# Performance work log

Measured on AMD Instinct MI355X. Metric: run time of the kernel, lower is better.

Reference implementation:

```python
import jax, jax.numpy as jnp
import numpy as np

B, T, I, H, L = 32, 512, 1024, 1024, 2

def setup_inputs() -> dict:
    key = jax.random.key(0)
    ks = jax.random.split(key, 5)
    x = jax.random.normal(ks[0], (B, T, I), dtype=jnp.float32)
    # nn.Linear weight layout: [out_features, in_features] = [4H, in+H]
    scale0 = (6.0 / (4 * H + I + H)) ** 0.5  # xavier uniform bound
    scale1 = (6.0 / (4 * H + H + H)) ** 0.5
    W0 = jax.random.uniform(ks[1], (4 * H, I + H), minval=-scale0, maxval=scale0, dtype=jnp.float32)
    W1 = jax.random.uniform(ks[2], (4 * H, H + H), minval=-scale1, maxval=scale1, dtype=jnp.float32)
    # bias: zeros, with forget-gate slice (first H) set to 1, per reset_parameters
    b = jnp.zeros((4 * H,), dtype=jnp.float32).at[:H].set(1.0)
    return {"x": x, "W0": W0, "b0": b, "W1": W1, "b1": b}

def _cell(x_in, h_prev, c_prev, W, b):
    # combined:[B, in+H] @ W.T -> [B, 4H]
    gates = jnp.concatenate([x_in, h_prev], axis=1) @ W.T + b
    f, i, g, o = jnp.split(gates, 4, axis=1)
    f = jax.nn.sigmoid(f)
    i = jax.nn.sigmoid(i)
    g = jnp.tanh(g)
    o = jax.nn.sigmoid(o)
    c_next = f * c_prev + i * g
    h_next = o * jnp.tanh(c_next)
    return h_next, c_next

def reference(x, W0, b0, W1, b1):
    Ws = (W0, W1)
    bs = (b0, b1)
    x_t_major = jnp.transpose(x, (1, 0, 2))  # [T, B, I]
    h0 = jnp.zeros((L, B, H), dtype=x.dtype)
    c0 = jnp.zeros((L, B, H), dtype=x.dtype)

    def step(carry, x_t):
        h, c = carry
        inp = x_t
        hs, cs = [], []
        for l in range(L):
            h_new, c_new = _cell(inp, h[l], c[l], Ws[l], bs[l])
            hs.append(h_new)
            cs.append(c_new)
            inp = h_new  # dropout=0 -> identity between layers
        return (jnp.stack(hs), jnp.stack(cs)), inp

    (h_n, c_n), outs = jax.lax.scan(step, (h0, c0), x_t_major)
    outputs = jnp.transpose(outs, (1, 0, 2))  # batch_first
    return outputs, h_n, c_n
```

## Files before the change

### kernel.cpp

```cpp
#include <hip/hip_runtime.h>
#include <hip/hip_bf16.h>
#include <cstdint>
#include <cstddef>


typedef unsigned short ush;
typedef short bf16x8 __attribute__((ext_vector_type(8)));
typedef float f32x4 __attribute__((ext_vector_type(4)));
typedef int i32x4 __attribute__((ext_vector_type(4)));
typedef unsigned long long u64;

#define TT 512
#define NA 64
#define NB 128
#define RING 8

__device__ __forceinline__ ush f2bf(float f) {
  __hip_bfloat16 h = __float2bfloat16(f);
  return *reinterpret_cast<ush*>(&h);
}
__device__ __forceinline__ float sigm(float x) { return 1.f / (1.f + __expf(-x)); }

__device__ __forceinline__ unsigned int aload(const unsigned int* p) {
  return __hip_atomic_load(p, __ATOMIC_RELAXED, __HIP_MEMORY_SCOPE_AGENT);
}
__device__ __forceinline__ void astore(unsigned int* p, unsigned int v) {
  __hip_atomic_store(p, v, __ATOMIC_RELAXED, __HIP_MEMORY_SCOPE_AGENT);
}

__global__ __launch_bounds__(256) void cast_w1k(const float* __restrict__ W,
                                                ush* __restrict__ Wb, int off) {
  int j = blockIdx.x;
  int k = threadIdx.x * 4;
  float4 v = *(const float4*)(W + (size_t)j * 2048 + off + k);
  ushort4 o;
  o.x = f2bf(v.x); o.y = f2bf(v.y); o.z = f2bf(v.z); o.w = f2bf(v.w);
  *(ushort4*)(Wb + (size_t)j * 1024 + k) = o;
}

__global__ __launch_bounds__(256) void swz0(const float* __restrict__ W,
                                            ush* __restrict__ D) {
  int n = blockIdx.x * 256 + threadIdx.x;
  int lane = n & 63, ch = (n >> 6) & 15, w = (n >> 10) & 7, i = n >> 13;
  int l15 = lane & 15, quad = lane >> 4, g = w & 3, kh = w >> 2;
  int row = g * 1024 + i * 16 + l15;
  int col = 1024 + kh * 512 + ch * 32 + quad * 8;
  const float* src = W + (size_t)row * 2048 + col;
  float4 v0 = ((const float4*)src)[0];
  float4 v1 = ((const float4*)src)[1];
  ushort4 o0, o1;
  o0.x = f2bf(v0.x); o0.y = f2bf(v0.y); o0.z = f2bf(v0.z); o0.w = f2bf(v0.w);
  o1.x = f2bf(v1.x); o1.y = f2bf(v1.y); o1.z = f2bf(v1.z); o1.w = f2bf(v1.w);
  *(ushort4*)(D + (size_t)n * 8) = o0;
  *(ushort4*)(D + (size_t)n * 8 + 4) = o1;
}

__global__ __launch_bounds__(256) void swz1(const float* __restrict__ W,
                                            ush* __restrict__ D) {
  int n = blockIdx.x * 256 + threadIdx.x;
  int lane = n & 63, ch = (n >> 6) & 15, w = (n >> 10) & 7, j = n >> 13;
  int l15 = lane & 15, quad = lane >> 4, rh = w & 1, kq = w >> 1;
  int r32 = rh * 16 + l15;
  int row = (r32 >> 3) * 1024 + j * 8 + (r32 & 7);
  int col = kq * 512 + ch * 32 + quad * 8;
  const float* src = W + (size_t)row * 2048 + col;
  float4 v0 = ((const float4*)src)[0];
  float4 v1 = ((const float4*)src)[1];
  ushort4 o0, o1;
  o0.x = f2bf(v0.x); o0.y = f2bf(v0.y); o0.z = f2bf(v0.z); o0.w = f2bf(v0.w);
  o1.x = f2bf(v1.x); o1.y = f2bf(v1.y); o1.z = f2bf(v1.z); o1.w = f2bf(v1.w);
  *(ushort4*)(D + (size_t)n * 8) = o0;
  *(ushort4*)(D + (size_t)n * 8 + 4) = o1;
}

__global__ __launch_bounds__(256) void zeroreg(uint4* __restrict__ p) {
  p[blockIdx.x * 256 + threadIdx.x] = uint4{0, 0, 0, 0};
}

__global__ __launch_bounds__(256) void gemm128(
    const float* __restrict__ xA, const ush* __restrict__ Wb,
    const float* __restrict__ bias, float* __restrict__ G, int t0) {
  __shared__ ush As[128][88];
  __shared__ ush Bs[128][88];
  int tid = threadIdx.x;
  int bn = blockIdx.x, bm = blockIdx.y;
  int srow = tid >> 1;
  int shalf = (tid & 1) * 32;
  int lane = tid & 63, quad = lane >> 4, l15 = lane & 15;
  int w = tid >> 6;
  int m_base = (w >> 1) * 64, n_base = (w & 1) * 64;

  int r = bm * 128 + srow;
  const float* axf = xA + ((size_t)(r & 31) * TT + t0 + (r >> 5)) * 1024;
  const ush* wrow = Wb + (size_t)(bn * 128 + srow) * 1024;

  f32x4 acc[4][4];
#pragma unroll
  for (int i = 0; i < 4; ++i)
#pragma unroll
    for (int j = 0; j < 4; ++j) acc[i][j] = f32x4{0.f, 0.f, 0.f, 0.f};

  for (int k0 = 0; k0 < 1024; k0 += 64) {
    {
      const float* p = axf + k0 + shalf;
      ush* d = &As[srow][shalf];
#pragma unroll
      for (int s = 0; s < 8; ++s) {
        float4 v = ((const float4*)p)[s];
        ushort4 o;
        o.x = f2bf(v.x); o.y = f2bf(v.y); o.z = f2bf(v.z); o.w = f2bf(v.w);
        ((ushort4*)d)[s] = o;
      }
    }
    {
      const uint4* p = (const uint4*)(wrow + k0 + shalf);
      uint4* d = (uint4*)&Bs[srow][shalf];
#pragma unroll
      for (int s = 0; s < 4; ++s) d[s] = p[s];
    }
    __syncthreads();
#pragma unroll
    for (int kc = 0; kc < 2; ++kc) {
      bf16x8 af[4], bf_[4];
#pragma unroll
      for (int i = 0; i < 4; ++i)
        af[i] = *(const bf16x8*)&As[m_base + i * 16 + l15][kc * 32 + quad * 8];
#pragma unroll
      for (int j = 0; j < 4; ++j)
        bf_[j] = *(const bf16x8*)&Bs[n_base + j * 16 + l15][kc * 32 + quad * 8];
#pragma unroll
      for (int i = 0; i < 4; ++i)
#pragma unroll
        for (int j = 0; j < 4; ++j)
          acc[i][j] = __builtin_amdgcn_mfma_f32_16x16x32_bf16(af[i], bf_[j],
                                                              acc[i][j], 0, 0, 0);
    }
    __syncthreads();
  }

#pragma unroll
  for (int j = 0; j < 4; ++j) {
    int col = bn * 128 + n_base + j * 16 + l15;
    float bj = bias[col];
#pragma unroll
    for (int i = 0; i < 4; ++i) {
      int row = bm * 128 + m_base + i * 16 + quad * 4;
#pragma unroll
      for (int reg = 0; reg < 4; ++reg)
        G[(size_t)(row + reg) * 4096 + col] = acc[i][j][reg] + bj;
    }
  }
}

__global__ __launch_bounds__(512, 2) void lstm_persist(
    const float* __restrict__ G0, const ush* __restrict__ Wsw0,
    const ush* __restrict__ Wsw1, const float* __restrict__ b1,
    ush* __restrict__ h0r, ush* __restrict__ h1r,
    unsigned int* __restrict__ flg,
    float* __restrict__ cst, float* __restrict__ OUT,
    float* __restrict__ hno, float* __restrict__ cno,
    int t0, int Tc, int last) {
  __shared__ ush hbuf[65536];
  __shared__ float pg[8][32][20];
  char* hb = (char*)hbuf;

  int tid = threadIdx.x;
  int bid = blockIdx.x;
  int w = tid >> 6, lane = tid & 63, quad = lane >> 4, l15 = lane & 15;
  unsigned int* prog0 = flg;
  unsigned int* prog1 = flg + 1024;

  if (bid < NA) {
    int c0 = bid * 16;
    const ush* wp = Wsw0 + ((size_t)bid * 8 + w) * 8192 + (size_t)lane * 8;
    bf16x8 wreg[16];
#pragma unroll
    for (int ch = 0; ch < 16; ++ch) wreg[ch] = *(const bf16x8*)(wp + ch * 512);
#pragma unroll
    for (int ch = 0; ch < 16; ++ch) asm volatile("" : "+v"(wreg[ch]));
    int b = tid >> 4, c = tid & 15;
    int ci = b * 1024 + c0 + c;
    float creg = (t0 > 0) ? cst[ci] : 0.f;
    int m1c = t0;
    int kbase = (w >> 2) * 1024 + quad * 16;
    int x0 = (l15 & 7) << 4;
    const char* a0p = hb + l15 * 2048;
    const char* a1p = hb + (16 + l15) * 2048;

    for (int s = 0; s < Tc; ++s) {
      int t = t0 + s;
      const float* grow = G0 + (size_t)(s * 32 + b) * 4096 + c0 + c;
      float g0v = grow[0], g1v = grow[1024], g2v = grow[2048], g3v = grow[3072];
      if (w == 0) {
        if ((int)aload(&prog0[lane * 16]) < t) {
          do { __builtin_amdgcn_s_sleep(1); } while ((int)aload(&prog0[lane * 16]) < t);
        }
        while (m1c < t - (RING - 1)) {
          int m = (int)aload(&prog1[lane * 16]);
          m = min(m, (int)aload(&prog1[(64 + lane) * 16]));
#pragma unroll
          for (int d = 1; d < 64; d <<= 1) m = min(m, __shfl_xor(m, d));
          m1c = m;
          if (m1c < t - (RING - 1)) __builtin_amdgcn_s_sleep(2);
        }
      }
      __syncthreads();
      {
        const char* src = (const char*)h0r + (size_t)((t - 1) & (RING - 1)) * 65536;
        i32x4 r_[8];
#pragma unroll
        for (int s2 = 0; s2 < 8; ++s2) {
          int gi = s2 * 512 + tid;
          asm volatile("global_load_dwordx4 %0, %1, off sc1"
                       : "=v"(r_[s2]) : "v"(src + (size_t)gi * 16));
        }
        asm volatile("s_waitcnt vmcnt(0)" ::: "memory");
        __builtin_amdgcn_sched_barrier(0);
#pragma unroll
        for (int s2 = 0; s2 < 8; ++s2) {
          int gi = s2 * 512 + tid;
          int r = gi >> 7, kb = (gi & 127) * 16;
          *(i32x4*)(hb + r * 2048 + (kb ^ ((r & 7) << 4))) = r_[s2];
        }
      }
      __syncthreads();
      f32x4 acc0 = {0.f, 0.f, 0.f, 0.f}, acc1 = {0.f, 0.f, 0.f, 0.f};
#pragma unroll
      for (int ch = 0; ch < 16; ++ch) {
        int kb = kbase + ch * 64;
        bf16x8 a0 = *(const bf16x8*)(a0p + (kb ^ x0));
        bf16x8 a1 = *(const bf16x8*)(a1p + (kb ^ x0));
        acc0 = __builtin_amdgcn_mfma_f32_16x16x32_bf16(a0, wreg[ch], acc0, 0, 0, 0);
        acc1 = __builtin_amdgcn_mfma_f32_16x16x32_bf16(a1, wreg[ch], acc1, 0, 0, 0);
      }
#pragma unroll
      for (int reg = 0; reg < 4; ++reg) {
        pg[w][quad * 4 + reg][l15] = acc0[reg];
        pg[w][16 + quad * 4 + reg][l15] = acc1[reg];
      }
      __syncthreads();
      float s0 = g0v + pg[0][b][c] + pg[4][b][c];
      float s1 = g1v + pg[1][b][c] + pg[5][b][c];
      float s2 = g2v + pg[2][b][c] + pg[6][b][c];
      float s3 = g3v + pg[3][b][c] + pg[7][b][c];
      float fg = sigm(s0), ig = sigm(s1), gv = tanhf(s2), og = sigm(s3);
      creg = fg * creg + ig * gv;
      float hnv = og * tanhf(creg);
      float ho = __shfl_xor(hnv, 1);
      unsigned int pk = (unsigned int)f2bf(hnv) | ((unsigned int)f2bf(ho) << 16);
      unsigned int pk2 = __shfl_xor(pk, 2);
      u64 d0 = (u64)pk | ((u64)pk2 << 32);
      u64 d1 = (u64)__shfl_xor((long long)d0, 4);
      if ((tid & 7) == 0) {
        i32x4 v;
        v.x = (int)d0; v.y = (int)(d0 >> 32);
        v.z = (int)d1; v.w = (int)(d1 >> 32);
        char* dp = (char*)(h0r + (size_t)(t & (RING - 1)) * 32768 +
                           (size_t)b * 1024 + c0 + c);
        asm volatile("global_store_dwordx4 %0, %1, off sc1"
                     :: "v"(dp), "v"(v) : "memory");
      }
      if (t == TT - 1) hno[ci] = hnv;
      asm volatile("s_waitcnt vmcnt(0)" ::: "memory");
      __syncthreads();
      if (tid == 0) astore(&prog0[bid * 16], (unsigned int)(t + 1));
    }
    cst[ci] = creg;
    if (last) cno[ci] = creg;
  } else {
    int jb = bid - NA;
    int c0b = jb * 8;
    const ush* wp = Wsw1 + ((size_t)jb * 8 + w) * 8192 + (size_t)lane * 8;
    bf16x8 wreg[16];
#pragma unroll
    for (int ch = 0; ch < 16; ++ch) wreg[ch] = *(const bf16x8*)(wp + ch * 512);
#pragma unroll
    for (int ch = 0; ch < 16; ++ch) asm volatile("" : "+v"(wreg[ch]));
    bool pw = tid < 256;
    int b = tid >> 3, cc = tid & 7;
    int ci = b * 1024 + c0b + cc;
    float creg = 0.f;
    float biasr[4] = {0.f, 0.f, 0.f, 0.f};
    if (pw) {
      creg = (t0 > 0) ? cst[32768 + ci] : 0.f;
#pragma unroll
      for (int g = 0; g < 4; ++g) biasr[g] = b1[g * 1024 + c0b + cc];
    }
    int kq = w >> 1;
    int boff = (kq < 2) ? 0 : 65536;
    int kbase = (kq & 1) * 1024 + quad * 16;
    int x0 = (l15 & 7) << 4;
    const char* a0p = hb + boff + l15 * 2048;
    const char* a1p = a0p + 16 * 2048;

    for (int s = 0; s < Tc; ++s) {
      int t = t0 + s;
      if (w == 0) {
        if ((int)aload(&prog0[lane * 16]) < t + 1) {
          do { __builtin_amdgcn_s_sleep(1); } while ((int)aload(&prog0[lane * 16]) < t + 1);
        }
      }
      __syncthreads();
      i32x4 r0_[8];
      {
        const char* src = (const char*)h0r + (size_t)(t & (RING - 1)) * 65536;
#pragma unroll
        for (int s2 = 0; s2 < 8; ++s2) {
          int gi = s2 * 512 + tid;
          asm volatile("global_load_dwordx4 %0, %1, off sc1"
                       : "=v"(r0_[s2]) : "v"(src + (size_t)gi * 16));
        }
      }
      if (w == 0) {
        while ((int)aload(&prog1[lane * 16]) < t ||
               (int)aload(&prog1[(64 + lane) * 16]) < t)
          __builtin_amdgcn_s_sleep(1);
      }
      __syncthreads();
      {
        const char* src = (const char*)h1r + (size_t)((t - 1) & (RING - 1)) * 65536;
        i32x4 r1_[8];
#pragma unroll
        for (int s2 = 0; s2 < 8; ++s2) {
          int gi = s2 * 512 + tid;
          asm volatile("global_load_dwordx4 %0, %1, off sc1"
                       : "=v"(r1_[s2]) : "v"(src + (size_t)gi * 16));
        }
        asm volatile("s_waitcnt vmcnt(0)" ::: "memory");
        __builtin_amdgcn_sched_barrier(0);
#pragma unroll
        for (int s2 = 0; s2 < 8; ++s2) {
          int gi = s2 * 512 + tid;
          int r = gi >> 7, kb = (gi & 127) * 16;
          *(i32x4*)(hb + r * 2048 + (kb ^ ((r & 7) << 4))) = r0_[s2];
          *(i32x4*)(hb + 65536 + r * 2048 + (kb ^ ((r & 7) << 4))) = r1_[s2];
        }
      }
      __syncthreads();
      f32x4 acc0 = {0.f, 0.f, 0.f, 0.f}, acc1 = {0.f, 0.f, 0.f, 0.f};
#pragma unroll
      for (int ch = 0; ch < 16; ++ch) {
        int kb = kbase + ch * 64;
        bf16x8 a0 = *(const bf16x8*)(a0p + (kb ^ x0));
        bf16x8 a1 = *(const bf16x8*)(a1p + (kb ^ x0));
        acc0 = __builtin_amdgcn_mfma_f32_16x16x32_bf16(a0, wreg[ch], acc0, 0, 0, 0);
        acc1 = __builtin_amdgcn_mfma_f32_16x16x32_bf16(a1, wreg[ch], acc1, 0, 0, 0);
      }
#pragma unroll
      for (int reg = 0; reg < 4; ++reg) {
        pg[w][quad * 4 + reg][l15] = acc0[reg];
        pg[w][16 + quad * 4 + reg][l15] = acc1[reg];
      }
      __syncthreads();
      float hnv = 0.f;
      if (pw) {
        float sg[4];
#pragma unroll
        for (int g = 0; g < 4; ++g) {
          int r = g * 8 + cc, rrh = r >> 4, ri = r & 15;
          sg[g] = biasr[g] + pg[rrh][b][ri] + pg[2 + rrh][b][ri] +
                  pg[4 + rrh][b][ri] + pg[6 + rrh][b][ri];
        }
        float fg = sigm(sg[0]), ig = sigm(sg[1]), gv = tanhf(sg[2]),
              og = sigm(sg[3]);
        creg = fg * creg + ig * gv;
        hnv = og * tanhf(creg);
        float ho = __shfl_xor(hnv, 1);
        unsigned int pk = (unsigned int)f2bf(hnv) | ((unsigned int)f2bf(ho) << 16);
        unsigned int pk2 = __shfl_xor(pk, 2);
        u64 d0 = (u64)pk | ((u64)pk2 << 32);
        u64 d1 = (u64)__shfl_xor((long long)d0, 4);
        if ((tid & 7) == 0) {
          i32x4 v;
          v.x = (int)d0; v.y = (int)(d0 >> 32);
          v.z = (int)d1; v.w = (int)(d1 >> 32);
          char* dp = (char*)(h1r + (size_t)(t & (RING - 1)) * 32768 +
                             (size_t)b * 1024 + c0b);
          asm volatile("global_store_dwordx4 %0, %1, off sc1"
                       :: "v"(dp), "v"(v) : "memory");
        }
      }
      asm volatile("s_waitcnt vmcnt(0)" ::: "memory");
      __syncthreads();
      if (tid == 0) astore(&prog1[jb * 16], (unsigned int)(t + 1));
      if (pw) {
        OUT[((size_t)b * TT + t) * 1024 + c0b + cc] = hnv;
        if (t == TT - 1) hno[32768 + ci] = hnv;
      }
    }
    if (pw) {
      cst[32768 + ci] = creg;
      if (last) cno[32768 + ci] = creg;
    }
  }
}

extern "C" void kernel_launch(void* const* d_in, const int* in_sizes, int n_in,
                              void* d_out, int out_size, void* d_ws, size_t ws_size,
                              hipStream_t stream) {
  const float* x = (const float*)d_in[0];
  const float* W0 = (const float*)d_in[1];
  const float* b0 = (const float*)d_in[2];
  const float* W1 = (const float*)d_in[3];
  const float* b1 = (const float*)d_in[4];
  float* OUT = (float*)d_out;

  int Tc = 4;
  {
    const int cand[8] = {512, 256, 128, 64, 32, 16, 8, 4};
    for (int i = 0; i < 8; ++i) {
      size_t need = 34881536ull + (size_t)cand[i] * 524288;
      if (need <= ws_size) { Tc = cand[i]; break; }
    }
  }
  char* ws = (char*)d_ws;
  ush* Wxb0 = (ush*)ws;
  ush* Wsw0 = (ush*)(ws + 8388608);
  ush* Wsw1 = (ush*)(ws + 16777216);
  ush* h0r = (ush*)(ws + 33554432);
  ush* h1r = (ush*)(ws + 34078720);
  unsigned int* flg = (unsigned int*)(ws + 34603008);
  float* cst = (float*)(ws + 34619392);
  float* G = (float*)(ws + 34881536);

  cast_w1k<<<4096, 256, 0, stream>>>(W0, Wxb0, 0);
  swz0<<<2048, 256, 0, stream>>>(W0, Wsw0);
  swz1<<<4096, 256, 0, stream>>>(W1, Wsw1);
  zeroreg<<<260, 256, 0, stream>>>((uint4*)(ws + 33554432));

  float* hnp = OUT + 16777216;
  float* cnp = OUT + 16777216 + 65536;
  dim3 ggrid(32, (unsigned)(Tc * 32 / 128));

  const int NCH = TT / Tc;
  for (int ch = 0; ch < NCH; ++ch) {
    int t0v = ch * Tc;
    int lastv = (ch == NCH - 1) ? 1 : 0;
    gemm128<<<ggrid, 256, 0, stream>>>(x, Wxb0, b0, G, t0v);
    void* pargs[14] = {(void*)&G,    (void*)&Wsw0, (void*)&Wsw1, (void*)&b1,
                       (void*)&h0r,  (void*)&h1r,  (void*)&flg,  (void*)&cst,
                       (void*)&OUT,  (void*)&hnp,  (void*)&cnp,  (void*)&t0v,
                       (void*)&Tc,   (void*)&lastv};
    hipLaunchCooperativeKernel((void*)lstm_persist, dim3(NA + NB), dim3(512),
                               pargs, 0, stream);
  }
}
```

Baseline: 2.876 ms.

## Split layer-1 input projection into separate workgroups to shorten the recurrent critical path

After: 2.683 ms. -6.7%, faster.

```diff
diff --git a/kernel.cpp b/kernel.cpp
--- a/kernel.cpp
+++ b/kernel.cpp
@@ -12,7 +12,6 @@
 
 #define TT 512
 #define NA 64
-#define NB 128
 #define RING 8
 
 __device__ __forceinline__ ush f2bf(float f) {
@@ -26,6 +25,9 @@
 }
 __device__ __forceinline__ void astore(unsigned int* p, unsigned int v) {
   __hip_atomic_store(p, v, __ATOMIC_RELAXED, __HIP_MEMORY_SCOPE_AGENT);
+}
+__device__ __forceinline__ float afload(const float* p) {
+  return __hip_atomic_load(p, __ATOMIC_RELAXED, __HIP_MEMORY_SCOPE_AGENT);
 }
 
 __global__ __launch_bounds__(256) void cast_w1k(const float* __restrict__ W,
@@ -38,13 +40,13 @@
   *(ushort4*)(Wb + (size_t)j * 1024 + k) = o;
 }
 
-__global__ __launch_bounds__(256) void swz0(const float* __restrict__ W,
-                                            ush* __restrict__ D) {
+__global__ __launch_bounds__(256) void swzW(const float* __restrict__ W,
+                                            ush* __restrict__ D, int coloff) {
   int n = blockIdx.x * 256 + threadIdx.x;
   int lane = n & 63, ch = (n >> 6) & 15, w = (n >> 10) & 7, i = n >> 13;
   int l15 = lane & 15, quad = lane >> 4, g = w & 3, kh = w >> 2;
   int row = g * 1024 + i * 16 + l15;
-  int col = 1024 + kh * 512 + ch * 32 + quad * 8;
+  int col = coloff + kh * 512 + ch * 32 + quad * 8;
   const float* src = W + (size_t)row * 2048 + col;
   float4 v0 = ((const float4*)src)[0];
   float4 v1 = ((const float4*)src)[1];
@@ -55,14 +57,14 @@
   *(ushort4*)(D + (size_t)n * 8 + 4) = o1;
 }
 
-__global__ __launch_bounds__(256) void swz1(const float* __restrict__ W,
-                                            ush* __restrict__ D) {
+__global__ __launch_bounds__(256) void swz1h(const float* __restrict__ W,
+                                             ush* __restrict__ D) {
   int n = blockIdx.x * 256 + threadIdx.x;
-  int lane = n & 63, ch = (n >> 6) & 15, w = (n >> 10) & 7, j = n >> 13;
+  int lane = n & 63, ch = (n >> 6) & 7, w = (n >> 9) & 7, jb = n >> 12;
   int l15 = lane & 15, quad = lane >> 4, rh = w & 1, kq = w >> 1;
   int r32 = rh * 16 + l15;
-  int row = (r32 >> 3) * 1024 + j * 8 + (r32 & 7);
-  int col = kq * 512 + ch * 32 + quad * 8;
+  int row = (r32 >> 3) * 1024 + jb * 8 + (r32 & 7);
+  int col = 1024 + kq * 256 + ch * 32 + quad * 8;
   const float* src = W + (size_t)row * 2048 + col;
   float4 v0 = ((const float4*)src)[0];
   float4 v1 = ((const float4*)src)[1];
@@ -154,13 +156,14 @@
 
 __global__ __launch_bounds__(512, 2) void lstm_persist(
     const float* __restrict__ G0, const ush* __restrict__ Wsw0,
-    const ush* __restrict__ Wsw1, const float* __restrict__ b1,
-    ush* __restrict__ h0r, ush* __restrict__ h1r,
+    const ush* __restrict__ WswP, const ush* __restrict__ Wsw1h,
+    const float* __restrict__ b1,
+    ush* __restrict__ h0r, ush* __restrict__ h1r, float* __restrict__ Pr,
     unsigned int* __restrict__ flg,
     float* __restrict__ cst, float* __restrict__ OUT,
     float* __restrict__ hno, float* __restrict__ cno,
     int t0, int Tc, int last) {
-  __shared__ ush hbuf[65536];
+  __shared__ ush hbuf[32768];
   __shared__ float pg[8][32][20];
   char* hb = (char*)hbuf;
 
@@ -169,6 +172,7 @@
   int w = tid >> 6, lane = tid & 63, quad = lane >> 4, l15 = lane & 15;
   unsigned int* prog0 = flg;
   unsigned int* prog1 = flg + 1024;
+  unsigned int* progP = flg + 3072;
 
   if (bid < NA) {
     int c0 = bid * 16;
@@ -181,7 +185,7 @@
     int b = tid >> 4, c = tid & 15;
     int ci = b * 1024 + c0 + c;
     float creg = (t0 > 0) ? cst[ci] : 0.f;
-    int m1c = t0;
+    int mPc = t0;
     int kbase = (w >> 2) * 1024 + quad * 16;
     int x0 = (l15 & 7) << 4;
     const char* a0p = hb + l15 * 2048;
@@ -195,13 +199,12 @@
         if ((int)aload(&prog0[lane * 16]) < t) {
           do { __builtin_amdgcn_s_sleep(1); } while ((int)aload(&prog0[lane * 16]) < t);
         }
-        while (m1c < t - (RING - 1)) {
-          int m = (int)aload(&prog1[lane * 16]);
-          m = min(m, (int)aload(&prog1[(64 + lane) * 16]));
+        while (mPc < t - (RING - 1)) {
+          int m = (int)aload(&progP[lane * 16]);
 #pragma unroll
           for (int d = 1; d < 64; d <<= 1) m = min(m, __shfl_xor(m, d));
-          m1c = m;
-          if (m1c < t - (RING - 1)) __builtin_amdgcn_s_sleep(2);
+          mPc = m;
+          if (mPc < t - (RING - 1)) __builtin_amdgcn_s_sleep(2);
         }
       }
       __syncthreads();
@@ -267,15 +270,98 @@
     }
     cst[ci] = creg;
     if (last) cno[ci] = creg;
+  } else if (bid < 2 * NA) {
+    int p = bid - NA;
+    int c0 = p * 16;
+    const ush* wp = WswP + ((size_t)p * 8 + w) * 8192 + (size_t)lane * 8;
+    bf16x8 wreg[16];
+#pragma unroll
+    for (int ch = 0; ch < 16; ++ch) wreg[ch] = *(const bf16x8*)(wp + ch * 512);
+#pragma unroll
+    for (int ch = 0; ch < 16; ++ch) asm volatile("" : "+v"(wreg[ch]));
+    int b = tid >> 4, c = tid & 15;
+    int m1c = t0;
+    int kbase = (w >> 2) * 1024 + quad * 16;
+    int x0 = (l15 & 7) << 4;
+    const char* a0p = hb + l15 * 2048;
+    const char* a1p = hb + (16 + l15) * 2048;
+
+    for (int s = 0; s < Tc; ++s) {
+      int t = t0 + s;
+      if (w == 0) {
+        if ((int)aload(&prog0[lane * 16]) < t + 1) {
+          do { __builtin_amdgcn_s_sleep(1); } while ((int)aload(&prog0[lane * 16]) < t + 1);
+        }
+        while (m1c < t - (RING - 1)) {
+          int m = (int)aload(&prog1[lane * 16]);
+          m = min(m, (int)aload(&prog1[(64 + lane) * 16]));
+#pragma unroll
+          for (int d = 1; d < 64; d <<= 1) m = min(m, __shfl_xor(m, d));
+          m1c = m;
+          if (m1c < t - (RING - 1)) __builtin_amdgcn_s_sleep(2);
+        }
+      }
+      __syncthreads();
+      {
+        const char* src = (const char*)h0r + (size_t)(t & (RING - 1)) * 65536;
+        i32x4 r_[8];
+#pragma unroll
+        for (int s2 = 0; s2 < 8; ++s2) {
+          int gi = s2 * 512 + tid;
+          asm volatile("global_load_dwordx4 %0, %1, off sc1"
+                       : "=v"(r_[s2]) : "v"(src + (size_t)gi * 16));
+        }
+        asm volatile("s_waitcnt vmcnt(0)" ::: "memory");
+        __builtin_amdgcn_sched_barrier(0);
+#pragma unroll
+        for (int s2 = 0; s2 < 8; ++s2) {
+          int gi = s2 * 512 + tid;
+          int r = gi >> 7, kb = (gi & 127) * 16;
+          *(i32x4*)(hb + r * 2048 + (kb ^ ((r & 7) << 4))) = r_[s2];
+        }
+      }
+      __syncthreads();
+      f32x4 acc0 = {0.f, 0.f, 0.f, 0.f}, acc1 = {0.f, 0.f, 0.f, 0.f};
+#pragma unroll
+      for (int ch = 0; ch < 16; ++ch) {
+        int kb = kbase + ch * 64;
+        bf16x8 a0 = *(const bf16x8*)(a0p + (kb ^ x0));
+        bf16x8 a1 = *(const bf16x8*)(a1p + (kb ^ x0));
+        acc0 = __builtin_amdgcn_mfma_f32_16x16x32_bf16(a0, wreg[ch], acc0, 0, 0, 0);
+        acc1 = __builtin_amdgcn_mfma_f32_16x16x32_bf16(a1, wreg[ch], acc1, 0, 0, 0);
+      }
+#pragma unroll
+      for (int reg = 0; reg < 4; ++reg) {
+        pg[w][quad * 4 + reg][l15] = acc0[reg];
+        pg[w][16 + quad * 4 + reg][l15] = acc1[reg];
+      }
+      __syncthreads();
+      float s0 = pg[0][b][c] + pg[4][b][c];
+      float s1 = pg[1][b][c] + pg[5][b][c];
+      float s2 = pg[2][b][c] + pg[6][b][c];
+      float s3 = pg[3][b][c] + pg[7][b][c];
+      {
+        i32x4 v;
+        v.x = __float_as_int(s0); v.y = __float_as_int(s1);
+        v.z = __float_as_int(s2); v.w = __float_as_int(s3);
+        char* dp = (char*)Pr + (size_t)(t & (RING - 1)) * 524288 +
+                   (size_t)(b * 1024 + c0 + c) * 16;
+        asm volatile("global_store_dwordx4 %0, %1, off sc1"
+                     :: "v"(dp), "v"(v) : "memory");
+      }
+      asm volatile("s_waitcnt vmcnt(0)" ::: "memory");
+      __syncthreads();
+      if (tid == 0) astore(&progP[p * 16], (unsigned int)(t + 1));
+    }
   } else {
-    int jb = bid - NA;
+    int jb = bid - 2 * NA;
     int c0b = jb * 8;
-    const ush* wp = Wsw1 + ((size_t)jb * 8 + w) * 8192 + (size_t)lane * 8;
-    bf16x8 wreg[16];
-#pragma unroll
-    for (int ch = 0; ch < 16; ++ch) wreg[ch] = *(const bf16x8*)(wp + ch * 512);
-#pragma unroll
-    for (int ch = 0; ch < 16; ++ch) asm volatile("" : "+v"(wreg[ch]));
+    const ush* wp = Wsw1h + ((size_t)jb * 8 + w) * 4096 + (size_t)lane * 8;
+    bf16x8 wreg[8];
+#pragma unroll
+    for (int ch = 0; ch < 8; ++ch) wreg[ch] = *(const bf16x8*)(wp + ch * 512);
+#pragma unroll
+    for (int ch = 0; ch < 8; ++ch) asm volatile("" : "+v"(wreg[ch]));
     bool pw = tid < 256;
     int b = tid >> 3, cc = tid & 7;
     int ci = b * 1024 + c0b + cc;
@@ -287,29 +373,26 @@
       for (int g = 0; g < 4; ++g) biasr[g] = b1[g * 1024 + c0b + cc];
     }
     int kq = w >> 1;
-    int boff = (kq < 2) ? 0 : 65536;
-    int kbase = (kq & 1) * 1024 + quad * 16;
+    int kbase = kq * 512 + quad * 16;
     int x0 = (l15 & 7) << 4;
-    const char* a0p = hb + boff + l15 * 2048;
-    const char* a1p = a0p + 16 * 2048;
+    const char* a0p = hb + l15 * 2048;
+    const char* a1p = hb + (16 + l15) * 2048;
 
     for (int s = 0; s < Tc; ++s) {
       int t = t0 + s;
       if (w == 0) {
-        if ((int)aload(&prog0[lane * 16]) < t + 1) {
-          do { __builtin_amdgcn_s_sleep(1); } while ((int)aload(&prog0[lane * 16]) < t + 1);
-        }
-      }
-      __syncthreads();
-      i32x4 r0_[8];
-      {
-        const char* src = (const char*)h0r + (size_t)(t & (RING - 1)) * 65536;
-#pragma unroll
-        for (int s2 = 0; s2 < 8; ++s2) {
-          int gi = s2 * 512 + tid;
-          asm volatile("global_load_dwordx4 %0, %1, off sc1"
-                       : "=v"(r0_[s2]) : "v"(src + (size_t)gi * 16));
-        }
+        if ((int)aload(&progP[(jb >> 1) * 16]) < t + 1) {
+          do { __builtin_amdgcn_s_sleep(1); } while ((int)aload(&progP[(jb >> 1) * 16]) < t + 1);
+        }
+      }
+      __syncthreads();
+      float pf[4] = {0.f, 0.f, 0.f, 0.f};
+      if (pw) {
+        const float* pp = (const float*)((const char*)Pr +
+                          (size_t)(t & (RING - 1)) * 524288) +
+                          (size_t)(b * 1024 + c0b + cc) * 4;
+#pragma unroll
+        for (int g = 0; g < 4; ++g) pf[g] = afload(pp + g);
       }
       if (w == 0) {
         while ((int)aload(&prog1[lane * 16]) < t ||
@@ -332,14 +415,13 @@
         for (int s2 = 0; s2 < 8; ++s2) {
           int gi = s2 * 512 + tid;
           int r = gi >> 7, kb = (gi & 127) * 16;
-          *(i32x4*)(hb + r * 2048 + (kb ^ ((r & 7) << 4))) = r0_[s2];
-          *(i32x4*)(hb + 65536 + r * 2048 + (kb ^ ((r & 7) << 4))) = r1_[s2];
+          *(i32x4*)(hb + r * 2048 + (kb ^ ((r & 7) << 4))) = r1_[s2];
         }
       }
       __syncthreads();
       f32x4 acc0 = {0.f, 0.f, 0.f, 0.f}, acc1 = {0.f, 0.f, 0.f, 0.f};
 #pragma unroll
-      for (int ch = 0; ch < 16; ++ch) {
+      for (int ch = 0; ch < 8; ++ch) {
         int kb = kbase + ch * 64;
         bf16x8 a0 = *(const bf16x8*)(a0p + (kb ^ x0));
         bf16x8 a1 = *(const bf16x8*)(a1p + (kb ^ x0));
@@ -358,7 +440,7 @@
 #pragma unroll
         for (int g = 0; g < 4; ++g) {
           int r = g * 8 + cc, rrh = r >> 4, ri = r & 15;
-          sg[g] = biasr[g] + pg[rrh][b][ri] + pg[2 + rrh][b][ri] +
+          sg[g] = biasr[g] + pf[g] + pg[rrh][b][ri] + pg[2 + rrh][b][ri] +
                   pg[4 + rrh][b][ri] + pg[6 + rrh][b][ri];
         }
         float fg = sigm(sg[0]), ig = sigm(sg[1]), gv = tanhf(sg[2]),
@@ -409,24 +491,27 @@
   {
     const int cand[8] = {512, 256, 128, 64, 32, 16, 8, 4};
     for (int i = 0; i < 8; ++i) {
-      size_t need = 34881536ull + (size_t)cand[i] * 524288;
+      size_t need = 39075840ull + (size_t)cand[i] * 524288;
       if (need <= ws_size) { Tc = cand[i]; break; }
     }
   }
   char* ws = (char*)d_ws;
   ush* Wxb0 = (ush*)ws;
   ush* Wsw0 = (ush*)(ws + 8388608);
-  ush* Wsw1 = (ush*)(ws + 16777216);
+  ush* WswP = (ush*)(ws + 16777216);
+  ush* Wsw1h = (ush*)(ws + 25165824);
   ush* h0r = (ush*)(ws + 33554432);
   ush* h1r = (ush*)(ws + 34078720);
-  unsigned int* flg = (unsigned int*)(ws + 34603008);
-  float* cst = (float*)(ws + 34619392);
-  float* G = (float*)(ws + 34881536);
+  float* Pr = (float*)(ws + 34603008);
+  unsigned int* flg = (unsigned int*)(ws + 38797312);
+  float* cst = (float*)(ws + 38813696);
+  float* G = (float*)(ws + 39075840);
 
   cast_w1k<<<4096, 256, 0, stream>>>(W0, Wxb0, 0);
-  swz0<<<2048, 256, 0, stream>>>(W0, Wsw0);
-  swz1<<<4096, 256, 0, stream>>>(W1, Wsw1);
-  zeroreg<<<260, 256, 0, stream>>>((uint4*)(ws + 33554432));
+  swzW<<<2048, 256, 0, stream>>>(W0, Wsw0, 1024);
+  swzW<<<2048, 256, 0, stream>>>(W1, WswP, 0);
+  swz1h<<<2048, 256, 0, stream>>>(W1, Wsw1h);
+  zeroreg<<<1284, 256, 0, stream>>>((uint4*)(ws + 33554432));
 
   float* hnp = OUT + 16777216;
   float* cnp = OUT + 16777216 + 65536;
@@ -437,11 +522,13 @@
     int t0v = ch * Tc;
     int lastv = (ch == NCH - 1) ? 1 : 0;
     gemm128<<<ggrid, 256, 0, stream>>>(x, Wxb0, b0, G, t0v);
-    void* pargs[14] = {(void*)&G,    (void*)&Wsw0, (void*)&Wsw1, (void*)&b1,
-                       (void*)&h0r,  (void*)&h1r,  (void*)&flg,  (void*)&cst,
-                       (void*)&OUT,  (void*)&hnp,  (void*)&cnp,  (void*)&t0v,
-                       (void*)&Tc,   (void*)&lastv};
-    hipLaunchCooperativeKernel((void*)lstm_persist, dim3(NA + NB), dim3(512),
+    void* pargs[16] = {(void*)&G,     (void*)&Wsw0, (void*)&WswP,
+                       (void*)&Wsw1h, (void*)&b1,   (void*)&h0r,
+                       (void*)&h1r,   (void*)&Pr,   (void*)&flg,
+                       (void*)&cst,   (void*)&OUT,  (void*)&hnp,
+                       (void*)&cnp,   (void*)&t0v,  (void*)&Tc,
+                       (void*)&lastv};
+    hipLaunchCooperativeKernel((void*)lstm_persist, dim3(4 * NA), dim3(512),
                                pargs, 0, stream);
   }
 }
```
